# Performance work log

Hardware: AMD Instinct MI355X
Metric: run time of the kernel (lower is better)

Reference implementation:

```python
import jax, jax.numpy as jnp
import numpy as np


def _rope_2d(x, h, w, c, base=10000.0):
    """Apply 2D rotary embedding to x of shape (b, h, w, c)."""
    k_max = c // 4  # c // (2 * num_spatial_dims)
    theta = 1.0 / (base ** (jnp.arange(k_max, dtype=jnp.float32) / k_max))  # (k_max,)
    ang_h = jnp.arange(h, dtype=jnp.float32)[:, None] * theta               # (h, k_max)
    ang_w = jnp.arange(w, dtype=jnp.float32)[:, None] * theta               # (w, k_max)
    # torch meshgrid(indexing='ij') then cat -> [h-angles, w-angles] along last dim
    angles = jnp.concatenate([
        jnp.broadcast_to(ang_h[:, None, :], (h, w, k_max)),
        jnp.broadcast_to(ang_w[None, :, :], (h, w, k_max)),
    ], axis=-1)                                                             # (h, w, c//2)
    cos, sin = jnp.cos(angles), jnp.sin(angles)
    xr = x.reshape(*x.shape[:-1], c // 2, 2)
    re, im = xr[..., 0], xr[..., 1]
    out = jnp.stack([cos * re - sin * im, sin * re + cos * im], axis=-1)
    return out.reshape(x.shape)


def _depthwise_conv3x3(x_nchw, kernel, bias):
    # kernel: (C, 1, 3, 3), groups = C
    c = x_nchw.shape[1]
    out = jax.lax.conv_general_dilated(
        x_nchw, kernel, window_strides=(1, 1), padding='SAME',
        feature_group_count=c, dimension_numbers=('NCHW', 'OIHW', 'NCHW'))
    return out + bias[None, :, None, None]


def setup_inputs() -> dict:
    key = jax.random.key(0)
    ks = jax.random.split(key, 8)
    b, h, w, c = 8, 120, 160, 96
    n = h * w
    inp = {
        'x1': jax.random.normal(ks[0], (b, n, c), dtype=jnp.float32),
        'x2': jax.random.normal(ks[1], (b, n, c), dtype=jnp.float32),
        'Wqk': jax.random.normal(ks[2], (2 * c, c), dtype=jnp.float32) * 0.02,
        'bqk': jnp.zeros((2 * c,), dtype=jnp.float32),
        'Wv': jax.random.normal(ks[3], (c, c), dtype=jnp.float32) * 0.02,
        'bv': jnp.zeros((c,), dtype=jnp.float32),
        'lepe_w': jax.random.normal(ks[4], (c, 1, 3, 3), dtype=jnp.float32) * 0.1,
        'lepe_b': jnp.zeros((c,), dtype=jnp.float32),
        'h': h,
        'w': w,
    }
    return inp


def reference(x1, x2, Wqk, bqk, Wv, bv, lepe_w, lepe_b, h, w):
    b, n, c = x1.shape
    num_heads = 3
    d = c // num_heads

    def qk_feat(x):
        qk = x @ Wqk.T + bqk                      # (b, n, 2c)
        q, k = qk[..., :c], qk[..., c:]
        return jax.nn.elu(q) + 1.0, jax.nn.elu(k) + 1.0

    q1, k1 = qk_feat(x1)
    q2, k2 = qk_feat(x2)

    def heads(t):  # (b, n, c) -> (b, H, n, d)
        return t.reshape(b, n, num_heads, d).transpose(0, 2, 1, 3)

    q1r = heads(_rope_2d(q1.reshape(b, h, w, c), h, w, c).reshape(b, n, c))
    k1r = heads(_rope_2d(k1.reshape(b, h, w, c), h, w, c).reshape(b, n, c))
    q2r = heads(_rope_2d(q2.reshape(b, h, w, c), h, w, c).reshape(b, n, c))
    k2r = heads(_rope_2d(k2.reshape(b, h, w, c), h, w, c).reshape(b, n, c))
    q1h, k1h, q2h, k2h = heads(q1), heads(k1), heads(q2), heads(k2)

    v1 = heads(x1 @ Wv.T + bv)                    # (b, H, n, d)
    v2 = heads(x2 @ Wv.T + bv)

    # cross normalizers (non-rope q, mean of non-rope opposite k)
    z1 = 1.0 / (jnp.einsum('bhnd,bhd->bhn', q1h, k2h.mean(axis=2)) + 1e-6)
    z2 = 1.0 / (jnp.einsum('bhnd,bhd->bhn', q2h, k1h.mean(axis=2)) + 1e-6)

    inv_n = 1.0 / n
    kv2 = jnp.einsum('bhnd,bhne->bhde', k2r, v2) * inv_n  # (b, H, d, d)
    kv1 = jnp.einsum('bhnd,bhne->bhde', k1r, v1) * inv_n

    o1 = jnp.einsum('bhnd,bhde->bhne', q1r, kv2) * z1[..., None]
    o2 = jnp.einsum('bhnd,bhde->bhne', q2r, kv1) * z2[..., None]

    o1 = o1.transpose(0, 2, 1, 3).reshape(b, n, c)
    o2 = o2.transpose(0, 2, 1, 3).reshape(b, n, c)

    # lepe: depthwise conv residual on v (NCHW)
    v1_img = v1.transpose(0, 2, 1, 3).reshape(b, h, w, c).transpose(0, 3, 1, 2)
    v2_img = v2.transpose(0, 2, 1, 3).reshape(b, h, w, c).transpose(0, 3, 1, 2)
    o1 = o1 + _depthwise_conv3x3(v1_img, lepe_w, lepe_b).transpose(0, 2, 3, 1).reshape(b, n, c)
    o2 = o2 + _depthwise_conv3x3(v2_img, lepe_w, lepe_b).transpose(0, 2, 3, 1).reshape(b, n, c)

    x1_out = o1.transpose(0, 2, 1).reshape(b, c, h, w)
    x2_out = o2.transpose(0, 2, 1).reshape(b, c, h, w)
    return (x1_out, x2_out)
```

## Files before the change

### kernel.cpp

```cpp
#include <hip/hip_runtime.h>
#include <hip/hip_bf16.h>

constexpr int B_ = 8;
constexpr int H_ = 120;
constexpr int W_ = 160;
constexpr int N_ = H_ * W_;
constexpr int C_ = 96;

constexpr int GX1 = 75;
constexpr int TPB1 = 4;
constexpr int NT2 = N_ / 64;

typedef __attribute__((ext_vector_type(8))) short s16x8;
typedef __attribute__((ext_vector_type(4))) short s16x4;
typedef __attribute__((ext_vector_type(4))) float f32x4;

static __device__ inline unsigned short f2bf(float f) {
    unsigned u = __float_as_uint(f);
    return (unsigned short)((u + 0x7FFFu + ((u >> 16) & 1u)) >> 16);
}
static __device__ inline float bf2f(unsigned short h) {
    return __uint_as_float(((unsigned)h) << 16);
}
static __device__ inline void MFMA(f32x4& c, s16x8 a, s16x8 b) {
    c = __builtin_amdgcn_mfma_f32_16x16x32_bf16(a, b, c, 0, 0, 0);
}

__global__ void prep_kernel(const float* __restrict__ Wqk, const float* __restrict__ Wv,
                            unsigned short* __restrict__ wpack,
                            float* __restrict__ csS, float* __restrict__ snS) {
    int idx = blockIdx.x * 256 + threadIdx.x;
    if (idx < 6720) {
        int j, pos;
        if (idx < 2880) { j = idx / 120; pos = idx - j * 120; }
        else { int t = idx - 2880; j = t / 160; pos = t - j * 160; }
        float theta = expf(-(float)j * (9.210340371976184f / 24.0f));
        float s, c;
        sincosf((float)pos * theta, &s, &c);
        csS[idx] = c;
        snS[idx] = s;
    } else if (idx < 6720 + 3456) {
        int i = idx - 6720;
        int s3 = i / 1152, rem = i - s3 * 1152;
        int cT = rem >> 6, lane = rem & 63;
        int col = cT * 16 + (lane & 15), k0 = s3 * 32 + 8 * (lane >> 4);
        const float* wp = (col < 192) ? (Wqk + col * 96 + k0) : (Wv + (col - 192) * 96 + k0);
        f32x4 wa = *(const f32x4*)wp;
        f32x4 wb = *(const f32x4*)(wp + 4);
        s16x8 wf;
        wf[0] = (short)f2bf(wa[0]); wf[1] = (short)f2bf(wa[1]);
        wf[2] = (short)f2bf(wa[2]); wf[3] = (short)f2bf(wa[3]);
        wf[4] = (short)f2bf(wb[0]); wf[5] = (short)f2bf(wb[1]);
        wf[6] = (short)f2bf(wb[2]); wf[7] = (short)f2bf(wb[3]);
        *(s16x8*)&wpack[i * 8] = wf;
    }
}

__global__ __launch_bounds__(256, 2)
void pass1_kernel(const float* __restrict__ x1, const float* __restrict__ x2,
                  const unsigned short* __restrict__ wpack,
                  const float* __restrict__ bqk, const float* __restrict__ bv,
                  const float* __restrict__ csS, const float* __restrict__ snS,
                  unsigned short* __restrict__ qbuf, unsigned short* __restrict__ vbuf,
                  float* __restrict__ kvpart, float* __restrict__ kmpart)
{
    __shared__ alignas(16) unsigned short Wl[27648];
    __shared__ alignas(16) unsigned short kTl[6144];
    __shared__ alignas(16) unsigned short vTl[6144];

    const int tid = threadIdx.x;
    const int l = tid & 63, w = tid >> 6;
    const int gx = blockIdx.x, b = blockIdx.y, s = blockIdx.z;
    const float* x = s ? x2 : x1;
    const int sb = s * B_ + b;

    for (int i = tid; i < 3456; i += 256)
        *(s16x8*)&Wl[i * 8] = *(const s16x8*)&wpack[i * 8];

    float biasv[18];
#pragma unroll
    for (int cT = 0; cT < 18; ++cT) {
        int col = cT * 16 + (l & 15);
        biasv[cT] = (col < 192) ? bqk[col] : bv[col - 192];
    }
    f32x4 kvacc[3] = {};
    float kmacc[6] = {};

    auto xload = [&](int n0t, f32x4* dst) {
        const float* xr = x + ((size_t)b * N_ + n0t + 16 * w + (l & 15)) * 96 + 8 * (l >> 4);
#pragma unroll
        for (int s3 = 0; s3 < 3; ++s3) {
            dst[2 * s3]     = *(const f32x4*)(xr + s3 * 32);
            dst[2 * s3 + 1] = *(const f32x4*)(xr + s3 * 32 + 4);
        }
    };
    f32x4 xcur[6], xnxt[6];
    xload(gx * TPB1 * 64, xcur);
    __syncthreads();

    for (int t = 0; t < TPB1; ++t) {
        const int n0 = (gx * TPB1 + t) * 64;
        const int r0 = 16 * w + 4 * (l >> 4);
        if (t + 1 < TPB1) xload(n0 + 64, xnxt);
        f32x4 acc[18] = {};
#pragma unroll
        for (int s3 = 0; s3 < 3; ++s3) {
            f32x4 xa = xcur[2 * s3], xb = xcur[2 * s3 + 1];
            s16x8 af;
            af[0] = (short)f2bf(xa[0]); af[1] = (short)f2bf(xa[1]);
            af[2] = (short)f2bf(xa[2]); af[3] = (short)f2bf(xa[3]);
            af[4] = (short)f2bf(xb[0]); af[5] = (short)f2bf(xb[1]);
            af[6] = (short)f2bf(xb[2]); af[7] = (short)f2bf(xb[3]);
#pragma unroll
            for (int cT = 0; cT < 18; ++cT) {
                s16x8 bf = *(const s16x8*)&Wl[((s3 * 18 + cT) * 64 + l) * 8];
                MFMA(acc[cT], af, bf);
            }
        }
        const int nr = n0 + r0;
        const int ih = nr / 160, iw0 = nr - ih * 160;
        f32x4 c4a[6], s4a[6];
#pragma unroll
        for (int j6 = 0; j6 < 3; ++j6) {
            int p = j6 * 8 + ((l & 15) >> 1);
            float c = csS[p * 120 + ih], sv = snS[p * 120 + ih];
            c4a[j6][0] = c; c4a[j6][1] = c; c4a[j6][2] = c; c4a[j6][3] = c;
            s4a[j6][0] = sv; s4a[j6][1] = sv; s4a[j6][2] = sv; s4a[j6][3] = sv;
        }
#pragma unroll
        for (int j6 = 3; j6 < 6; ++j6) {
            int pw = (j6 - 3) * 8 + ((l & 15) >> 1);
            c4a[j6] = *(const f32x4*)&csS[2880 + pw * 160 + iw0];
            s4a[j6] = *(const f32x4*)&snS[2880 + pw * 160 + iw0];
        }
        __syncthreads();

        unsigned short* qb = qbuf + ((size_t)sb * N_ + n0) * 96;
        unsigned short* vb = vbuf + ((size_t)sb * N_ + n0) * 96;
#pragma unroll
        for (int cT = 0; cT < 6; ++cT) {
#pragma unroll
            for (int i2 = 0; i2 < 4; ++i2) {
                float q = acc[cT][i2] + biasv[cT];
                q = (q > 0.f) ? q + 1.f : __expf(q);
                qb[(size_t)(r0 + i2) * 96 + cT * 16 + (l & 15)] = f2bf(q);
            }
        }
#pragma unroll
        for (int cT = 6; cT < 12; ++cT) {
            f32x4 c4 = c4a[cT - 6];
            f32x4 s4 = s4a[cT - 6];
            float colsum = 0.f;
            s16x4 pk;
#pragma unroll
            for (int i2 = 0; i2 < 4; ++i2) {
                float k = acc[cT][i2] + biasv[cT];
                k = (k > 0.f) ? k + 1.f : __expf(k);
                colsum += k;
                float kpart = __shfl_xor(k, 1, 64);
                float kr = (l & 1) ? fmaf(s4[i2], kpart, c4[i2] * k)
                                   : fmaf(-s4[i2], kpart, c4[i2] * k);
                pk[i2] = (short)f2bf(kr);
            }
            int chunk = ((r0 >> 5) * 6 + (cT - 6)) * 64 + ((r0 >> 3) & 3) * 16 + (l & 15);
            *(s16x4*)&kTl[chunk * 8 + (r0 & 7)] = pk;
            colsum += __shfl_xor(colsum, 16, 64);
            colsum += __shfl_xor(colsum, 32, 64);
            kmacc[cT - 6] += colsum;
        }
#pragma unroll
        for (int cT = 12; cT < 18; ++cT) {
            s16x4 pv;
#pragma unroll
            for (int i2 = 0; i2 < 4; ++i2) {
                float v = acc[cT][i2] + biasv[cT];
                unsigned short hv = f2bf(v);
                pv[i2] = (short)hv;
                vb[(size_t)(r0 + i2) * 96 + (cT - 12) * 16 + (l & 15)] = hv;
            }
            int chunk = ((r0 >> 5) * 6 + (cT - 12)) * 64 + ((r0 >> 3) & 3) * 16 + (l & 15);
            *(s16x4*)&vTl[chunk * 8 + (r0 & 7)] = pv;
        }
        __syncthreads();
#pragma unroll
        for (int j = 0; j < 3; ++j) {
            int f = w + 4 * j;
            int h = f >> 2, dT = (f >> 1) & 1, eT = f & 1;
#pragma unroll
            for (int ks = 0; ks < 2; ++ks) {
                s16x8 a = *(const s16x8*)&kTl[(((ks * 6 + (h * 2 + dT)) << 6) + l) * 8];
                s16x8 bb = *(const s16x8*)&vTl[(((ks * 6 + (h * 2 + eT)) << 6) + l) * 8];
                MFMA(kvacc[j], a, bb);
            }
        }
        if (t + 1 < TPB1) {
#pragma unroll
            for (int i = 0; i < 6; ++i) xcur[i] = xnxt[i];
        }
    }
    float* kvp = kvpart + ((size_t)sb * GX1 + gx) * 3072;
#pragma unroll
    for (int j = 0; j < 3; ++j) {
        int f = w + 4 * j;
        int h = f >> 2, dT = (f >> 1) & 1, eT = f & 1;
#pragma unroll
        for (int i2 = 0; i2 < 4; ++i2)
            kvp[h * 1024 + (dT * 16 + 4 * (l >> 4) + i2) * 32 + eT * 16 + (l & 15)] = kvacc[j][i2];
    }
    if (l < 16) {
        float* kmp = kmpart + ((size_t)((size_t)sb * GX1 + gx) * 4 + w) * 96;
#pragma unroll
        for (int j6 = 0; j6 < 6; ++j6) kmp[j6 * 16 + l] = kmacc[j6];
    }
}

__global__ void reduce_kernel(const float* __restrict__ kvpart, const float* __restrict__ kmpart,
                              float* __restrict__ kvbuf, float* __restrict__ kmbuf)
{
    int idx = blockIdx.x * 256 + threadIdx.x;
    const float invN = 1.0f / (float)N_;
    if (idx < 16 * 768) {
        int sb = idx / 768, e4 = idx - sb * 768;
        f32x4 acc = {0.f, 0.f, 0.f, 0.f};
        for (int g = 0; g < GX1; ++g) {
            f32x4 vv = *(const f32x4*)&kvpart[((size_t)sb * GX1 + g) * 3072 + e4 * 4];
            acc[0] += vv[0]; acc[1] += vv[1]; acc[2] += vv[2]; acc[3] += vv[3];
        }
        acc[0] *= invN; acc[1] *= invN; acc[2] *= invN; acc[3] *= invN;
        *(f32x4*)&kvbuf[(size_t)sb * 3072 + e4 * 4] = acc;
    } else if (idx < 16 * 768 + 16 * 96) {
        int j = idx - 16 * 768;
        int sb = j / 96, ch = j - sb * 96;
        float acc = 0.f;
        for (int g = 0; g < GX1 * 4; ++g) acc += kmpart[((size_t)sb * GX1 * 4 + g) * 96 + ch];
        kmbuf[j] = acc * invN;
    }
}

__global__ __launch_bounds__(256, 5)
void pass2_kernel(const unsigned short* __restrict__ qbuf, const unsigned short* __restrict__ vbuf,
                  const float* __restrict__ kvbuf, const float* __restrict__ kmbuf,
                  const float* __restrict__ csS, const float* __restrict__ snS,
                  const float* __restrict__ lw, const float* __restrict__ lb,
                  float* __restrict__ out)
{
    __shared__ alignas(16) char pbuf[25344];
    unsigned short* kvh = (unsigned short*)pbuf;
    float* osmT = (float*)pbuf;
    __shared__ float zsh[192];
    __shared__ float lwL[864], lbL[96];

    const int tid = threadIdx.x, l = tid & 63, w = tid >> 6;
    const int orig = blockIdx.x;
    const int xcd = orig & 7, i8 = orig >> 3;
    const int tile = (xcd < 4 ? xcd * 38 : 152 + (xcd - 4) * 37) + i8;
    const int b = blockIdx.y, s = blockIdx.z, so = 1 - s;
    const int n0 = tile * 64;
    const int sb = s * B_ + b, sbo = so * B_ + b;

    const float* kvsrc = kvbuf + (size_t)sbo * 3072;
    for (int i = tid; i < 3072; i += 256) {
        float vkv = kvsrc[i];
        int h = i >> 10, d = (i >> 5) & 31, e = i & 31;
        kvh[(h * 32 + e) * 40 + d] = f2bf(vkv);
    }
    for (int i = tid; i < 864; i += 256) lwL[i] = lw[i];
    if (tid < 96) lbL[tid] = lb[tid];

    const int qrow = n0 + 16 * w + (l & 15);
    const int ihq = qrow / 160, iwq = qrow - ihq * 160;
    const unsigned short* qr = qbuf + ((size_t)sb * N_ + qrow) * 96 + 8 * (l >> 4);
    const float* kmp = kmbuf + (size_t)sbo * 96 + 8 * (l >> 4);
    s16x8 qf[3];
    float zv[3];
#pragma unroll
    for (int h = 0; h < 3; ++h) {
        qf[h] = *(const s16x8*)&qr[h * 32];
        f32x4 km0 = *(const f32x4*)&kmp[h * 32];
        f32x4 km1 = *(const f32x4*)&kmp[h * 32 + 4];
        float zp = 0.f;
#pragma unroll
        for (int e = 0; e < 4; ++e) zp += bf2f((unsigned short)qf[h][e]) * km0[e];
#pragma unroll
        for (int e = 0; e < 4; ++e) zp += bf2f((unsigned short)qf[h][4 + e]) * km1[e];
        zp += __shfl_xor(zp, 16, 64);
        zp += __shfl_xor(zp, 32, 64);
        zv[h] = zp;
    }
    if (l < 16) {
#pragma unroll
        for (int h = 0; h < 3; ++h)
            zsh[h * 64 + 16 * w + l] = 1.f / (zv[h] + 1e-6f);
    }
    s16x8 af[3];
#pragma unroll
    for (int h = 0; h < 3; ++h) {
#pragma unroll
        for (int j = 0; j < 4; ++j) {
            int p = h * 16 + 4 * (l >> 4) + j;
            float c, sv;
            if (p < 24) { c = csS[p * 120 + ihq]; sv = snS[p * 120 + ihq]; }
            else { c = csS[2880 + (p - 24) * 160 + iwq]; sv = snS[2880 + (p - 24) * 160 + iwq]; }
            float re = bf2f((unsigned short)qf[h][2 * j]);
            float im = bf2f((unsigned short)qf[h][2 * j + 1]);
            af[h][2 * j]     = (short)f2bf(c * re - sv * im);
            af[h][2 * j + 1] = (short)f2bf(sv * re + c * im);
        }
    }
    __syncthreads();
    f32x4 oac[3][2] = {};
#pragma unroll
    for (int h = 0; h < 3; ++h) {
#pragma unroll
        for (int eT = 0; eT < 2; ++eT) {
            int rowb = (h * 32 + eT * 16 + (l & 15)) * 40 + 8 * (l >> 4);
            MFMA(oac[h][eT], af[h], *(const s16x8*)&kvh[rowb]);
        }
    }
    __syncthreads();
#pragma unroll
    for (int h = 0; h < 3; ++h) {
#pragma unroll
        for (int i2 = 0; i2 < 4; ++i2) {
            int row = 16 * w + 4 * (l >> 4) + i2;
            float z = zsh[h * 64 + row];
            osmT[(h * 32 + (l & 15)) * 66 + row] = oac[h][0][i2] * z;
            osmT[(h * 32 + 16 + (l & 15)) * 66 + row] = oac[h][1][i2] * z;
        }
    }
    __syncthreads();
    const unsigned short* vb = vbuf + (size_t)sb * (size_t)N_ * 96;
#pragma unroll
    for (int it = 0; it < 3; ++it) {
        int oct = it * 256 + tid;
        int r = oct / 12, c8 = oct - r * 12;
        int ch0 = c8 * 8;
        int npos = n0 + r, ih = npos / 160, iw = npos - ih * 160;
        float a[8];
#pragma unroll
        for (int e = 0; e < 8; ++e) a[e] = lbL[ch0 + e];
#pragma unroll
        for (int ky = 0; ky < 3; ++ky) {
            int ih2 = ih + ky - 1;
            if ((unsigned)ih2 >= 120u) continue;
#pragma unroll
            for (int kx = 0; kx < 3; ++kx) {
                int iw2 = iw + kx - 1;
                if ((unsigned)iw2 >= 160u) continue;
                s16x8 vv = *(const s16x8*)&vb[((size_t)ih2 * 160 + iw2) * 96 + ch0];
#pragma unroll
                for (int e = 0; e < 8; ++e)
                    a[e] = fmaf(bf2f((unsigned short)vv[e]), lwL[(ch0 + e) * 9 + ky * 3 + kx], a[e]);
            }
        }
#pragma unroll
        for (int e = 0; e < 8; ++e) osmT[(ch0 + e) * 66 + r] += a[e];
    }
    __syncthreads();
    float* ob = out + (size_t)sb * 96 * N_ + n0;
#pragma unroll
    for (int it = 0; it < 6; ++it) {
        int qq = it * 256 + tid;
        int r4 = (qq & 15) * 4, ch = qq >> 4;
        f32x4 vv;
        vv[0] = osmT[ch * 66 + r4];
        vv[1] = osmT[ch * 66 + r4 + 1];
        vv[2] = osmT[ch * 66 + r4 + 2];
        vv[3] = osmT[ch * 66 + r4 + 3];
        *(f32x4*)&ob[(size_t)ch * N_ + r4] = vv;
    }
}

extern "C" void kernel_launch(void* const* d_in, const int* in_sizes, int n_in,
                              void* d_out, int out_size, void* d_ws, size_t ws_size,
                              hipStream_t stream)
{
    const float* x1  = (const float*)d_in[0];
    const float* x2  = (const float*)d_in[1];
    const float* Wqk = (const float*)d_in[2];
    const float* bqk = (const float*)d_in[3];
    const float* Wv  = (const float*)d_in[4];
    const float* bv  = (const float*)d_in[5];
    const float* lw  = (const float*)d_in[6];
    const float* lb  = (const float*)d_in[7];
    float* out = (float*)d_out;

    char* ws = (char*)d_ws;
    size_t off = 0;
    auto alloc = [&](size_t bytes) -> void* {
        void* p = ws + off;
        off = (off + bytes + 255) & ~(size_t)255;
        return p;
    };
    unsigned short* qbuf = (unsigned short*)alloc(2ull * B_ * N_ * 96 * 2);
    unsigned short* vbuf = (unsigned short*)alloc(2ull * B_ * N_ * 96 * 2);
    float* kvpart = (float*)alloc(16ull * GX1 * 3072 * 4);
    float* kmpart = (float*)alloc(16ull * GX1 * 4 * 96 * 4);
    float* kvbuf  = (float*)alloc(16ull * 3072 * 4);
    float* kmbuf  = (float*)alloc(16ull * 96 * 4);
    unsigned short* wpack = (unsigned short*)alloc(3456ull * 8 * 2);
    float* csS = (float*)alloc(6720 * 4);
    float* snS = (float*)alloc(6720 * 4);

    hipLaunchKernelGGL(prep_kernel, dim3((6720 + 3456 + 255) / 256), dim3(256), 0, stream,
                       Wqk, Wv, wpack, csS, snS);
    hipLaunchKernelGGL(pass1_kernel, dim3(GX1, B_, 2), dim3(256), 0, stream,
                       x1, x2, wpack, bqk, bv, csS, snS, qbuf, vbuf, kvpart, kmpart);
    hipLaunchKernelGGL(reduce_kernel, dim3((16 * 768 + 16 * 96 + 255) / 256), dim3(256), 0, stream,
                       kvpart, kmpart, kvbuf, kmbuf);
    hipLaunchKernelGGL(pass2_kernel, dim3(NT2, B_, 2), dim3(256), 0, stream,
                       qbuf, vbuf, kvbuf, kmbuf, csS, snS, lw, lb, out);
}
```

Measured before the change: 201.4 us.

## Accumulate k^T v per wave in registers instead of via LDS transpose

Each wave now computes its share of the k^T v product directly from its own register fragments, using zero-padded 16x16x16 MFMAs. This removes the kTl/vTl shared-memory staging and the two per-tile barriers. The 18-tile projection accumulator is split into two 9-tile passes to cut register pressure, and the x prefetch double buffer is removed. Partial kv results from the four waves are summed through LDS once at the end of the block. In exchange, the kv MFMAs do half-empty work, and global-load latency is no longer hidden by the prefetch.

```diff
diff --git a/kernel.cpp b/kernel.cpp
--- a/kernel.cpp
+++ b/kernel.cpp
@@ -65,8 +65,6 @@
                   float* __restrict__ kvpart, float* __restrict__ kmpart)
 {
     __shared__ alignas(16) unsigned short Wl[27648];
-    __shared__ alignas(16) unsigned short kTl[6144];
-    __shared__ alignas(16) unsigned short vTl[6144];
 
     const int tid = threadIdx.x;
     const int l = tid & 63, w = tid >> 6;
@@ -83,130 +81,153 @@
         int col = cT * 16 + (l & 15);
         biasv[cT] = (col < 192) ? bqk[col] : bv[col - 192];
     }
-    f32x4 kvacc[3] = {};
+    f32x4 kvacc[12] = {};
     float kmacc[6] = {};
-
-    auto xload = [&](int n0t, f32x4* dst) {
-        const float* xr = x + ((size_t)b * N_ + n0t + 16 * w + (l & 15)) * 96 + 8 * (l >> 4);
-#pragma unroll
-        for (int s3 = 0; s3 < 3; ++s3) {
-            dst[2 * s3]     = *(const f32x4*)(xr + s3 * 32);
-            dst[2 * s3 + 1] = *(const f32x4*)(xr + s3 * 32 + 4);
-        }
-    };
-    f32x4 xcur[6], xnxt[6];
-    xload(gx * TPB1 * 64, xcur);
-    __syncthreads();
+    __syncthreads();
+
+    const int r0 = 16 * w + 4 * (l >> 4);
 
     for (int t = 0; t < TPB1; ++t) {
         const int n0 = (gx * TPB1 + t) * 64;
-        const int r0 = 16 * w + 4 * (l >> 4);
-        if (t + 1 < TPB1) xload(n0 + 64, xnxt);
-        f32x4 acc[18] = {};
-#pragma unroll
-        for (int s3 = 0; s3 < 3; ++s3) {
-            f32x4 xa = xcur[2 * s3], xb = xcur[2 * s3 + 1];
-            s16x8 af;
-            af[0] = (short)f2bf(xa[0]); af[1] = (short)f2bf(xa[1]);
-            af[2] = (short)f2bf(xa[2]); af[3] = (short)f2bf(xa[3]);
-            af[4] = (short)f2bf(xb[0]); af[5] = (short)f2bf(xb[1]);
-            af[6] = (short)f2bf(xb[2]); af[7] = (short)f2bf(xb[3]);
-#pragma unroll
-            for (int cT = 0; cT < 18; ++cT) {
-                s16x8 bf = *(const s16x8*)&Wl[((s3 * 18 + cT) * 64 + l) * 8];
-                MFMA(acc[cT], af, bf);
-            }
-        }
         const int nr = n0 + r0;
         const int ih = nr / 160, iw0 = nr - ih * 160;
-        f32x4 c4a[6], s4a[6];
-#pragma unroll
-        for (int j6 = 0; j6 < 3; ++j6) {
-            int p = j6 * 8 + ((l & 15) >> 1);
-            float c = csS[p * 120 + ih], sv = snS[p * 120 + ih];
-            c4a[j6][0] = c; c4a[j6][1] = c; c4a[j6][2] = c; c4a[j6][3] = c;
-            s4a[j6][0] = sv; s4a[j6][1] = sv; s4a[j6][2] = sv; s4a[j6][3] = sv;
-        }
-#pragma unroll
-        for (int j6 = 3; j6 < 6; ++j6) {
-            int pw = (j6 - 3) * 8 + ((l & 15) >> 1);
-            c4a[j6] = *(const f32x4*)&csS[2880 + pw * 160 + iw0];
-            s4a[j6] = *(const f32x4*)&snS[2880 + pw * 160 + iw0];
-        }
-        __syncthreads();
-
+
+        const float* xrow = x + ((size_t)b * N_ + n0 + 16 * w + (l & 15)) * 96 + 8 * (l >> 4);
+        s16x8 af[3];
+#pragma unroll
+        for (int s3 = 0; s3 < 3; ++s3) {
+            f32x4 xa = *(const f32x4*)(xrow + s3 * 32);
+            f32x4 xb = *(const f32x4*)(xrow + s3 * 32 + 4);
+            s16x8 a;
+            a[0] = (short)f2bf(xa[0]); a[1] = (short)f2bf(xa[1]);
+            a[2] = (short)f2bf(xa[2]); a[3] = (short)f2bf(xa[3]);
+            a[4] = (short)f2bf(xb[0]); a[5] = (short)f2bf(xb[1]);
+            a[6] = (short)f2bf(xb[2]); a[7] = (short)f2bf(xb[3]);
+            af[s3] = a;
+        }
         unsigned short* qb = qbuf + ((size_t)sb * N_ + n0) * 96;
         unsigned short* vb = vbuf + ((size_t)sb * N_ + n0) * 96;
-#pragma unroll
-        for (int cT = 0; cT < 6; ++cT) {
-#pragma unroll
-            for (int i2 = 0; i2 < 4; ++i2) {
-                float q = acc[cT][i2] + biasv[cT];
-                q = (q > 0.f) ? q + 1.f : __expf(q);
-                qb[(size_t)(r0 + i2) * 96 + cT * 16 + (l & 15)] = f2bf(q);
-            }
-        }
-#pragma unroll
-        for (int cT = 6; cT < 12; ++cT) {
-            f32x4 c4 = c4a[cT - 6];
-            f32x4 s4 = s4a[cT - 6];
-            float colsum = 0.f;
-            s16x4 pk;
-#pragma unroll
-            for (int i2 = 0; i2 < 4; ++i2) {
-                float k = acc[cT][i2] + biasv[cT];
-                k = (k > 0.f) ? k + 1.f : __expf(k);
-                colsum += k;
-                float kpart = __shfl_xor(k, 1, 64);
-                float kr = (l & 1) ? fmaf(s4[i2], kpart, c4[i2] * k)
-                                   : fmaf(-s4[i2], kpart, c4[i2] * k);
-                pk[i2] = (short)f2bf(kr);
-            }
-            int chunk = ((r0 >> 5) * 6 + (cT - 6)) * 64 + ((r0 >> 3) & 3) * 16 + (l & 15);
-            *(s16x4*)&kTl[chunk * 8 + (r0 & 7)] = pk;
-            colsum += __shfl_xor(colsum, 16, 64);
-            colsum += __shfl_xor(colsum, 32, 64);
-            kmacc[cT - 6] += colsum;
-        }
-#pragma unroll
-        for (int cT = 12; cT < 18; ++cT) {
-            s16x4 pv;
-#pragma unroll
-            for (int i2 = 0; i2 < 4; ++i2) {
-                float v = acc[cT][i2] + biasv[cT];
-                unsigned short hv = f2bf(v);
-                pv[i2] = (short)hv;
-                vb[(size_t)(r0 + i2) * 96 + (cT - 12) * 16 + (l & 15)] = hv;
-            }
-            int chunk = ((r0 >> 5) * 6 + (cT - 12)) * 64 + ((r0 >> 3) & 3) * 16 + (l & 15);
-            *(s16x4*)&vTl[chunk * 8 + (r0 & 7)] = pv;
-        }
-        __syncthreads();
-#pragma unroll
-        for (int j = 0; j < 3; ++j) {
-            int f = w + 4 * j;
-            int h = f >> 2, dT = (f >> 1) & 1, eT = f & 1;
-#pragma unroll
-            for (int ks = 0; ks < 2; ++ks) {
-                s16x8 a = *(const s16x8*)&kTl[(((ks * 6 + (h * 2 + dT)) << 6) + l) * 8];
-                s16x8 bb = *(const s16x8*)&vTl[(((ks * 6 + (h * 2 + eT)) << 6) + l) * 8];
-                MFMA(kvacc[j], a, bb);
-            }
-        }
-        if (t + 1 < TPB1) {
-#pragma unroll
-            for (int i = 0; i < 6; ++i) xcur[i] = xnxt[i];
-        }
-    }
+        s16x4 pkk[6], pvv[6];
+
+        {
+            f32x4 acc[9] = {};
+#pragma unroll
+            for (int s3 = 0; s3 < 3; ++s3)
+#pragma unroll
+                for (int j = 0; j < 9; ++j)
+                    MFMA(acc[j], af[s3], *(const s16x8*)&Wl[((s3 * 18 + j) * 64 + l) * 8]);
+#pragma unroll
+            for (int j = 0; j < 6; ++j) {
+#pragma unroll
+                for (int i2 = 0; i2 < 4; ++i2) {
+                    float q = acc[j][i2] + biasv[j];
+                    q = (q > 0.f) ? q + 1.f : __expf(q);
+                    qb[(size_t)(r0 + i2) * 96 + j * 16 + (l & 15)] = f2bf(q);
+                }
+            }
+#pragma unroll
+            for (int j6 = 0; j6 < 3; ++j6) {
+                int j = 6 + j6;
+                int p = j6 * 8 + ((l & 15) >> 1);
+                float cc = csS[p * 120 + ih], ss = snS[p * 120 + ih];
+                float colsum = 0.f;
+                s16x4 pk;
+#pragma unroll
+                for (int i2 = 0; i2 < 4; ++i2) {
+                    float k = acc[j][i2] + biasv[j];
+                    k = (k > 0.f) ? k + 1.f : __expf(k);
+                    colsum += k;
+                    float kpart = __shfl_xor(k, 1, 64);
+                    float kr = (l & 1) ? fmaf(ss, kpart, cc * k)
+                                       : fmaf(-ss, kpart, cc * k);
+                    pk[i2] = (short)f2bf(kr);
+                }
+                pkk[j6] = pk;
+                colsum += __shfl_xor(colsum, 16, 64);
+                colsum += __shfl_xor(colsum, 32, 64);
+                kmacc[j6] += colsum;
+            }
+        }
+        {
+            f32x4 acc[9] = {};
+#pragma unroll
+            for (int s3 = 0; s3 < 3; ++s3)
+#pragma unroll
+                for (int j = 0; j < 9; ++j)
+                    MFMA(acc[j], af[s3], *(const s16x8*)&Wl[((s3 * 18 + 9 + j) * 64 + l) * 8]);
+#pragma unroll
+            for (int j = 0; j < 3; ++j) {
+                int pw = j * 8 + ((l & 15) >> 1);
+                f32x4 c4 = *(const f32x4*)&csS[2880 + pw * 160 + iw0];
+                f32x4 s4 = *(const f32x4*)&snS[2880 + pw * 160 + iw0];
+                float colsum = 0.f;
+                s16x4 pk;
+#pragma unroll
+                for (int i2 = 0; i2 < 4; ++i2) {
+                    float k = acc[j][i2] + biasv[9 + j];
+                    k = (k > 0.f) ? k + 1.f : __expf(k);
+                    colsum += k;
+                    float kpart = __shfl_xor(k, 1, 64);
+                    float kr = (l & 1) ? fmaf(s4[i2], kpart, c4[i2] * k)
+                                       : fmaf(-s4[i2], kpart, c4[i2] * k);
+                    pk[i2] = (short)f2bf(kr);
+                }
+                pkk[3 + j] = pk;
+                colsum += __shfl_xor(colsum, 16, 64);
+                colsum += __shfl_xor(colsum, 32, 64);
+                kmacc[3 + j] += colsum;
+            }
+#pragma unroll
+            for (int j = 3; j < 9; ++j) {
+                s16x4 pv;
+#pragma unroll
+                for (int i2 = 0; i2 < 4; ++i2) {
+                    float v = acc[j][i2] + biasv[9 + j];
+                    unsigned short hv = f2bf(v);
+                    pv[i2] = (short)hv;
+                    vb[(size_t)(r0 + i2) * 96 + (j - 3) * 16 + (l & 15)] = hv;
+                }
+                pvv[j - 3] = pv;
+            }
+        }
+#pragma unroll
+        for (int h = 0; h < 3; ++h) {
+            s16x8 Bv[2];
+#pragma unroll
+            for (int eT = 0; eT < 2; ++eT) {
+                s16x4 pv = pvv[h * 2 + eT];
+                Bv[eT][0] = pv[0]; Bv[eT][1] = pv[1]; Bv[eT][2] = pv[2]; Bv[eT][3] = pv[3];
+                Bv[eT][4] = 0; Bv[eT][5] = 0; Bv[eT][6] = 0; Bv[eT][7] = 0;
+            }
+#pragma unroll
+            for (int dT = 0; dT < 2; ++dT) {
+                s16x4 pk = pkk[h * 2 + dT];
+                s16x8 A;
+                A[0] = pk[0]; A[1] = pk[1]; A[2] = pk[2]; A[3] = pk[3];
+                A[4] = 0; A[5] = 0; A[6] = 0; A[7] = 0;
+#pragma unroll
+                for (int eT = 0; eT < 2; ++eT)
+                    MFMA(kvacc[(h * 2 + dT) * 2 + eT], A, Bv[eT]);
+            }
+        }
+    }
+    __syncthreads();
+    float* red = (float*)Wl;
+#pragma unroll
+    for (int h = 0; h < 3; ++h)
+#pragma unroll
+        for (int dT = 0; dT < 2; ++dT)
+#pragma unroll
+            for (int eT = 0; eT < 2; ++eT) {
+                f32x4 v4 = kvacc[(h * 2 + dT) * 2 + eT];
+#pragma unroll
+                for (int i2 = 0; i2 < 4; ++i2)
+                    red[w * 3072 + h * 1024 + (dT * 16 + 4 * (l >> 4) + i2) * 32 + eT * 16 + (l & 15)] = v4[i2];
+            }
+    __syncthreads();
     float* kvp = kvpart + ((size_t)sb * GX1 + gx) * 3072;
-#pragma unroll
-    for (int j = 0; j < 3; ++j) {
-        int f = w + 4 * j;
-        int h = f >> 2, dT = (f >> 1) & 1, eT = f & 1;
-#pragma unroll
-        for (int i2 = 0; i2 < 4; ++i2)
-            kvp[h * 1024 + (dT * 16 + 4 * (l >> 4) + i2) * 32 + eT * 16 + (l & 15)] = kvacc[j][i2];
-    }
+    for (int i = tid; i < 3072; i += 256)
+        kvp[i] = red[i] + red[3072 + i] + red[6144 + i] + red[9216 + i];
     if (l < 16) {
         float* kmp = kmpart + ((size_t)((size_t)sb * GX1 + gx) * 4 + w) * 96;
 #pragma unroll
```

Measured after the change: 381.0 us. 1.89x slower.

## Precompute transposed bf16 KV in reduce kernel and drop pass2 LDS staging

Applied to the files above, without the earlier changes.

The reduce kernel now writes the averaged KV state already transposed and converted to bf16, in the layout the pass2 MFMA B operand expects. pass2 loads the B fragments straight from global memory instead of converting and staging 3072 floats into LDS per block. The 1/z normalizers are broadcast with wavefront shuffles rather than shared memory, which removes two block barriers and shrinks LDS use, possibly raising occupancy. In exchange, the reduce kernel reads partials with strided non-vector loads, and pass2 issues uncoalesced global loads that rely on cache hits.

```diff
diff --git a/kernel.cpp b/kernel.cpp
--- a/kernel.cpp
+++ b/kernel.cpp
@@ -215,19 +215,23 @@
 }
 
 __global__ void reduce_kernel(const float* __restrict__ kvpart, const float* __restrict__ kmpart,
-                              float* __restrict__ kvbuf, float* __restrict__ kmbuf)
+                              unsigned short* __restrict__ kvT, float* __restrict__ kmbuf)
 {
     int idx = blockIdx.x * 256 + threadIdx.x;
     const float invN = 1.0f / (float)N_;
     if (idx < 16 * 768) {
-        int sb = idx / 768, e4 = idx - sb * 768;
-        f32x4 acc = {0.f, 0.f, 0.f, 0.f};
+        int sb = idx / 768, r = idx - sb * 768;
+        int h = r >> 8, d4 = (r >> 5) & 7, e = r & 31;
+        float a0 = 0.f, a1 = 0.f, a2 = 0.f, a3 = 0.f;
+        const float* src = kvpart + (size_t)sb * GX1 * 3072 + h * 1024 + e;
         for (int g = 0; g < GX1; ++g) {
-            f32x4 vv = *(const f32x4*)&kvpart[((size_t)sb * GX1 + g) * 3072 + e4 * 4];
-            acc[0] += vv[0]; acc[1] += vv[1]; acc[2] += vv[2]; acc[3] += vv[3];
-        }
-        acc[0] *= invN; acc[1] *= invN; acc[2] *= invN; acc[3] *= invN;
-        *(f32x4*)&kvbuf[(size_t)sb * 3072 + e4 * 4] = acc;
+            const float* p = src + (size_t)g * 3072 + d4 * 128;
+            a0 += p[0]; a1 += p[32]; a2 += p[64]; a3 += p[96];
+        }
+        s16x4 o;
+        o[0] = (short)f2bf(a0 * invN); o[1] = (short)f2bf(a1 * invN);
+        o[2] = (short)f2bf(a2 * invN); o[3] = (short)f2bf(a3 * invN);
+        *(s16x4*)&kvT[(size_t)sb * 3072 + (h * 32 + e) * 32 + d4 * 4] = o;
     } else if (idx < 16 * 768 + 16 * 96) {
         int j = idx - 16 * 768;
         int sb = j / 96, ch = j - sb * 96;
@@ -239,15 +243,12 @@
 
 __global__ __launch_bounds__(256, 5)
 void pass2_kernel(const unsigned short* __restrict__ qbuf, const unsigned short* __restrict__ vbuf,
-                  const float* __restrict__ kvbuf, const float* __restrict__ kmbuf,
+                  const unsigned short* __restrict__ kvT, const float* __restrict__ kmbuf,
                   const float* __restrict__ csS, const float* __restrict__ snS,
                   const float* __restrict__ lw, const float* __restrict__ lb,
                   float* __restrict__ out)
 {
-    __shared__ alignas(16) char pbuf[25344];
-    unsigned short* kvh = (unsigned short*)pbuf;
-    float* osmT = (float*)pbuf;
-    __shared__ float zsh[192];
+    __shared__ alignas(16) float osmT[96 * 66];
     __shared__ float lwL[864], lbL[96];
 
     const int tid = threadIdx.x, l = tid & 63, w = tid >> 6;
@@ -258,12 +259,6 @@
     const int n0 = tile * 64;
     const int sb = s * B_ + b, sbo = so * B_ + b;
 
-    const float* kvsrc = kvbuf + (size_t)sbo * 3072;
-    for (int i = tid; i < 3072; i += 256) {
-        float vkv = kvsrc[i];
-        int h = i >> 10, d = (i >> 5) & 31, e = i & 31;
-        kvh[(h * 32 + e) * 40 + d] = f2bf(vkv);
-    }
     for (int i = tid; i < 864; i += 256) lwL[i] = lw[i];
     if (tid < 96) lbL[tid] = lb[tid];
 
@@ -272,7 +267,7 @@
     const unsigned short* qr = qbuf + ((size_t)sb * N_ + qrow) * 96 + 8 * (l >> 4);
     const float* kmp = kmbuf + (size_t)sbo * 96 + 8 * (l >> 4);
     s16x8 qf[3];
-    float zv[3];
+    float zinv[3];
 #pragma unroll
     for (int h = 0; h < 3; ++h) {
         qf[h] = *(const s16x8*)&qr[h * 32];
@@ -285,12 +280,7 @@
         for (int e = 0; e < 4; ++e) zp += bf2f((unsigned short)qf[h][4 + e]) * km1[e];
         zp += __shfl_xor(zp, 16, 64);
         zp += __shfl_xor(zp, 32, 64);
-        zv[h] = zp;
-    }
-    if (l < 16) {
-#pragma unroll
-        for (int h = 0; h < 3; ++h)
-            zsh[h * 64 + 16 * w + l] = 1.f / (zv[h] + 1e-6f);
+        zinv[h] = 1.f / (zp + 1e-6f);
     }
     s16x8 af[3];
 #pragma unroll
@@ -307,23 +297,22 @@
             af[h][2 * j + 1] = (short)f2bf(sv * re + c * im);
         }
     }
-    __syncthreads();
+    const unsigned short* kvb = kvT + (size_t)sbo * 3072;
     f32x4 oac[3][2] = {};
 #pragma unroll
     for (int h = 0; h < 3; ++h) {
 #pragma unroll
         for (int eT = 0; eT < 2; ++eT) {
-            int rowb = (h * 32 + eT * 16 + (l & 15)) * 40 + 8 * (l >> 4);
-            MFMA(oac[h][eT], af[h], *(const s16x8*)&kvh[rowb]);
-        }
-    }
-    __syncthreads();
+            s16x8 bfr = *(const s16x8*)&kvb[(h * 32 + eT * 16 + (l & 15)) * 32 + 8 * (l >> 4)];
+            MFMA(oac[h][eT], af[h], bfr);
+        }
+    }
 #pragma unroll
     for (int h = 0; h < 3; ++h) {
 #pragma unroll
         for (int i2 = 0; i2 < 4; ++i2) {
             int row = 16 * w + 4 * (l >> 4) + i2;
-            float z = zsh[h * 64 + row];
+            float z = __shfl(zinv[h], 4 * (l >> 4) + i2, 64);
             osmT[(h * 32 + (l & 15)) * 66 + row] = oac[h][0][i2] * z;
             osmT[(h * 32 + 16 + (l & 15)) * 66 + row] = oac[h][1][i2] * z;
         }
@@ -396,7 +385,7 @@
     unsigned short* vbuf = (unsigned short*)alloc(2ull * B_ * N_ * 96 * 2);
     float* kvpart = (float*)alloc(16ull * GX1 * 3072 * 4);
     float* kmpart = (float*)alloc(16ull * GX1 * 4 * 96 * 4);
-    float* kvbuf  = (float*)alloc(16ull * 3072 * 4);
+    unsigned short* kvT = (unsigned short*)alloc(16ull * 3072 * 2);
     float* kmbuf  = (float*)alloc(16ull * 96 * 4);
     unsigned short* wpack = (unsigned short*)alloc(3456ull * 8 * 2);
     float* csS = (float*)alloc(6720 * 4);
@@ -407,7 +396,7 @@
     hipLaunchKernelGGL(pass1_kernel, dim3(GX1, B_, 2), dim3(256), 0, stream,
                        x1, x2, wpack, bqk, bv, csS, snS, qbuf, vbuf, kvpart, kmpart);
     hipLaunchKernelGGL(reduce_kernel, dim3((16 * 768 + 16 * 96 + 255) / 256), dim3(256), 0, stream,
-                       kvpart, kmpart, kvbuf, kmbuf);
+                       kvpart, kmpart, kvT, kmbuf);
     hipLaunchKernelGGL(pass2_kernel, dim3(NT2, B_, 2), dim3(256), 0, stream,
-                       qbuf, vbuf, kvbuf, kmbuf, csS, snS, lw, lb, out);
-}
+                       qbuf, vbuf, kvT, kmbuf, csS, snS, lw, lb, out);
+}
```

Result: faster. 193.0 us (-4.1%).
